# Optimization experiments

Hardware: AMD Instinct MI355X
Metric: run time of the kernel (lower is better)

Reference implementation:

```python
import jax, jax.numpy as jnp
import numpy as np

D = 64
H = 256


def _directions(d):
    """Taylor-coefficient directions matching Bilaplacian._set_up_taylor_coefficients."""
    eye = np.eye(d, dtype=np.float32)
    dirs1 = 4.0 * eye                                   # (D, D): 4*e_i
    pairs_neq = np.array([(i, j) for i in range(d) for j in range(d) if i != j])
    dirs2 = 3.0 * eye[pairs_neq[:, 0]] + eye[pairs_neq[:, 1]]      # (D(D-1), D): 3 e_i + e_j
    pairs_lt = np.array([(i, j) for i in range(d) for j in range(i + 1, d)])
    dirs3 = 2.0 * eye[pairs_lt[:, 0]] + 2.0 * eye[pairs_lt[:, 1]]  # (D(D-1)/2, D): 2 e_i + 2 e_j
    return jnp.asarray(dirs1), jnp.asarray(dirs2), jnp.asarray(dirs3)


def setup_inputs() -> dict:
    key = jax.random.key(0)
    ks = jax.random.split(key, 7)
    x = jax.random.normal(ks[0], (D,), dtype=jnp.float32)
    W1 = jax.random.normal(ks[1], (H, D), dtype=jnp.float32) / np.sqrt(D)
    b1 = 0.1 * jax.random.normal(ks[2], (H,), dtype=jnp.float32)
    W2 = jax.random.normal(ks[3], (H, H), dtype=jnp.float32) / np.sqrt(H)
    b2 = 0.1 * jax.random.normal(ks[4], (H,), dtype=jnp.float32)
    W3 = jax.random.normal(ks[5], (1, H), dtype=jnp.float32) / np.sqrt(H)
    b3 = 0.1 * jax.random.normal(ks[6], (1,), dtype=jnp.float32)
    return {"x": x, "W1": W1, "b1": b1, "W2": W2, "b2": b2, "W3": W3, "b3": b3}


def _bilaplacian(x, W1, b1, W2, b2, W3, b3):
    d = x.shape[0]

    def f(z):
        h = jnp.tanh(W1 @ z + b1)
        h = jnp.tanh(W2 @ h + b2)
        return W3 @ h + b3  # (1,)

    def d4(v):
        # 4th directional derivative d^4/dt^4 f(x + t v) via Taylor-mode (nested jvp)
        g1 = lambda z: jax.jvp(f, (z,), (v,))[1]
        g2 = lambda z: jax.jvp(g1, (z,), (v,))[1]
        g3 = lambda z: jax.jvp(g2, (z,), (v,))[1]
        return jax.jvp(g3, (x,), (v,))[1]

    dirs1, dirs2, dirs3 = _directions(d)
    S1 = jax.vmap(d4)(dirs1).sum(0)
    S2 = jax.vmap(d4)(dirs2).sum(0)
    S3 = jax.vmap(d4)(dirs3).sum(0)
    # Polarization weights s.t. alpha*S1 + beta*S2 + gamma*S3 = sum_{i,j} d^4 f / dx_i^2 dx_j^2
    alpha = (1.0 + 13.0 * (d - 1) / 9.0) / 256.0
    beta = -1.0 / 36.0
    gamma = 5.0 / 96.0
    return alpha * S1 + beta * S2 + gamma * S3


def reference(x, W1, b1, W2, b2, W3, b3):
    return _bilaplacian(x, W1, b1, W2, b2, W3, b3)
```

## Files before the change

kernel.cpp:

```cpp
#include <hip/hip_runtime.h>
#include <hip/hip_bf16.h>


#define C_F    0
#define H0_F   1024
#define R2_F   1280
#define E_F    1536
#define Q_F    2560
#define S5_F   2816
#define U_F    3072
#define S3_F   3328
#define S4_F   3584
#define P2_F   3840
#define G_F    4096
#define P_F    69632

__global__ __launch_bounds__(256) void k1_kernel(
    const float* __restrict__ x, const float* __restrict__ W1,
    const float* __restrict__ b1, float* __restrict__ ws_f, int* __restrict__ cnt) {
    __shared__ __align__(16) float smem[2 * 64 * 68];
    int tid = threadIdx.x, b = blockIdx.x;

    if (b == 0) {
        float* xs = smem;
        if (tid < 64) xs[tid] = x[tid];
        __syncthreads();
        const float4* row = (const float4*)(W1 + tid * 64);
        const float4* xv4 = (const float4*)xs;
        float u0 = b1[tid], r2v = 0.f;
        #pragma unroll
        for (int k = 0; k < 16; k++) {
            float4 w = row[k], xv = xv4[k];
            u0  += w.x * xv.x + w.y * xv.y + w.z * xv.z + w.w * xv.w;
            r2v += w.x * w.x + w.y * w.y + w.z * w.z + w.w * w.w;
        }
        float T = tanhf(u0), s = 1.f - T * T;
        ws_f[C_F + tid]       = s;
        ws_f[C_F + 256 + tid] = -2.f * T * s;
        ws_f[C_F + 512 + tid] = s * (6.f * T * T - 2.f);
        ws_f[C_F + 768 + tid] = s * T * (16.f - 24.f * T * T);
        ws_f[H0_F + tid] = T;
        ws_f[R2_F + tid] = r2v;
        ws_f[U_F  + tid] = 0.f;
        ws_f[S3_F + tid] = 0.f;
        ws_f[S4_F + tid] = 0.f;
        if (tid == 0) *cnt = 0;
    } else {
        int tb = b - 1, nb = tb >> 2, pb = tb & 3;
        float* As = smem;
        float* Bs = smem + 64 * 68;
        for (int idx = tid; idx < 4096; idx += 256) {
            int r = idx >> 6, i = idx & 63;
            As[i * 68 + r] = W1[(nb * 64 + r) * 64 + i];
            Bs[i * 68 + r] = W1[(pb * 64 + r) * 64 + i];
        }
        __syncthreads();
        int r0 = (tid & 15) * 4, c0 = (tid >> 4) * 4;
        float a[4][4] = {};
        for (int i = 0; i < 64; i++) {
            float4 av = *(const float4*)&As[i * 68 + r0];
            float4 bv = *(const float4*)&Bs[i * 68 + c0];
            float ar[4] = {av.x, av.y, av.z, av.w};
            float br[4] = {bv.x, bv.y, bv.z, bv.w};
            #pragma unroll
            for (int rr = 0; rr < 4; rr++)
                #pragma unroll
                for (int cc = 0; cc < 4; cc++)
                    a[rr][cc] = fmaf(ar[rr], br[cc], a[rr][cc]);
        }
        float* G = ws_f + G_F;
        #pragma unroll
        for (int rr = 0; rr < 4; rr++)
            #pragma unroll
            for (int cc = 0; cc < 4; cc++)
                G[(nb * 64 + r0 + rr) * 256 + pb * 64 + c0 + cc] = a[rr][cc];
    }
}

__global__ __launch_bounds__(256) void k2_kernel(
    const float* __restrict__ W1, const float* __restrict__ W2,
    const float* __restrict__ b2, const float* __restrict__ W3,
    float* __restrict__ ws_f) {
    __shared__ __align__(16) float smem[13248];
    int tid = threadIdx.x, b = blockIdx.x;
    const float* c1g = ws_f + C_F;
    const float* c2g = ws_f + C_F + 256;
    const float* c4g = ws_f + C_F + 768;

    if (b < 8) {
        int m0 = b * 32;
        float* Wc = smem;
        float* Bc = smem + 64 * 34;
        float acc2[2][4] = {};
        int tm2 = (tid & 15) * 2, ti = (tid >> 4) * 4;
        for (int nc = 0; nc < 4; nc++) {
            __syncthreads();
            for (int idx = tid; idx < 2048; idx += 256) {
                int mm = idx >> 6, nn = idx & 63;
                Wc[nn * 34 + mm] = W2[(m0 + mm) * 256 + nc * 64 + nn];
            }
            for (int idx = tid; idx < 4096; idx += 256) {
                int nn = idx >> 6, ii = idx & 63, n = nc * 64 + nn;
                Bc[nn * 68 + ii] = c1g[n] * W1[n * 64 + ii];
            }
            __syncthreads();
            for (int nn = 0; nn < 64; nn++) {
                float2 a2 = *(const float2*)&Wc[nn * 34 + tm2];
                float4 b4 = *(const float4*)&Bc[nn * 68 + ti];
                float br[4] = {b4.x, b4.y, b4.z, b4.w};
                #pragma unroll
                for (int j = 0; j < 4; j++) {
                    acc2[0][j] = fmaf(a2.x, br[j], acc2[0][j]);
                    acc2[1][j] = fmaf(a2.y, br[j], acc2[1][j]);
                }
            }
        }
        float* P = ws_f + P_F;
        float s0 = 0.f, s1 = 0.f;
        #pragma unroll
        for (int j = 0; j < 4; j++) {
            P[(m0 + tm2) * 64 + ti + j]     = acc2[0][j];
            P[(m0 + tm2 + 1) * 64 + ti + j] = acc2[1][j];
            s0 += acc2[0][j] * acc2[0][j];
            s1 += acc2[1][j] * acc2[1][j];
        }
        __syncthreads();
        float* red = smem;
        red[tm2 * 16 + (tid >> 4)]       = s0;
        red[(tm2 + 1) * 16 + (tid >> 4)] = s1;
        __syncthreads();
        if (tid < 32) {
            float p = 0.f;
            #pragma unroll
            for (int g = 0; g < 16; g++) p += red[tid * 16 + g];
            ws_f[P2_F + m0 + tid] = p;
        }
    } else if (b < 12) {
        int m0 = (b - 8) * 64;
        float* Ws   = smem;
        float* h0s  = smem + 4160;
        float* aqs  = h0s + 256;
        float* a5s  = aqs + 256;
        float* part = a5s + 256;
        float r2v = ws_f[R2_F + tid];
        h0s[tid] = ws_f[H0_F + tid];
        aqs[tid] = c2g[tid] * r2v;
        a5s[tid] = c4g[tid] * r2v * r2v;
        int mm = tid & 63, nq = tid >> 6;
        float pv = 0.f, pq = 0.f, p5 = 0.f;
        for (int nc = 0; nc < 4; nc++) {
            __syncthreads();
            for (int idx = tid; idx < 4096; idx += 256) {
                int m2 = idx >> 6, nn = idx & 63;
                Ws[nn * 65 + m2] = W2[(m0 + m2) * 256 + nc * 64 + nn];
            }
            __syncthreads();
            #pragma unroll
            for (int k = 0; k < 16; k++) {
                int nn = nq * 16 + k, n = nc * 64 + nn;
                float wv = Ws[nn * 65 + mm];
                pv = fmaf(wv, h0s[n], pv);
                pq = fmaf(wv, aqs[n], pq);
                p5 = fmaf(wv, a5s[n], p5);
            }
        }
        part[nq * 64 + mm]       = pv;
        part[256 + nq * 64 + mm] = pq;
        part[512 + nq * 64 + mm] = p5;
        __syncthreads();
        if (tid < 64) {
            int m = m0 + tid;
            float v  = b2[m] + part[tid] + part[64 + tid] + part[128 + tid] + part[192 + tid];
            float q  = part[256 + tid] + part[320 + tid] + part[384 + tid] + part[448 + tid];
            float s5 = part[512 + tid] + part[576 + tid] + part[640 + tid] + part[704 + tid];
            float T2 = tanhf(v), s2 = 1.f - T2 * T2, w3 = W3[m];
            float* E = ws_f + E_F;
            E[m]       = w3 * s2;
            E[256 + m] = -2.f * w3 * T2 * s2;
            E[512 + m] = w3 * s2 * (6.f * T2 * T2 - 2.f);
            E[768 + m] = w3 * s2 * T2 * (16.f - 24.f * T2 * T2);
            ws_f[Q_F + m]  = q;
            ws_f[S5_F + m] = s5;
        }
    } else {
        int tb = b - 12, kb = tb >> 2, mb = tb & 3;
        float* As  = smem;
        float* Bs  = smem + 4352;
        float* W2k = smem + 8704;
        float* c2k = smem + 13056;
        for (int idx = tid; idx < 4096; idx += 256) {
            int a_ = idx >> 6, b_ = idx & 63;
            W2k[a_ * 68 + b_] = W2[(mb * 64 + a_) * 256 + kb * 64 + b_];
        }
        if (tid < 64) c2k[tid] = c2g[kb * 64 + tid];
        int r0 = (tid & 15) * 4, c0 = (tid >> 4) * 4;
        float a[4][4] = {};
        const float* G = ws_f + G_F;
        for (int nc = 0; nc < 4; nc++) {
            __syncthreads();
            float c2v = c2g[nc * 64 + (tid & 63)];
            for (int idx = tid; idx < 4096; idx += 256) {
                int a_ = idx >> 6, b_ = idx & 63;
                float gv = G[(kb * 64 + a_) * 256 + nc * 64 + b_];
                As[b_ * 68 + a_] = c2v * gv * gv;
                Bs[b_ * 68 + a_] = W2[(mb * 64 + a_) * 256 + nc * 64 + b_];
            }
            __syncthreads();
            for (int nn = 0; nn < 64; nn++) {
                float4 av = *(const float4*)&As[nn * 68 + r0];
                float4 bv = *(const float4*)&Bs[nn * 68 + c0];
                float ar[4] = {av.x, av.y, av.z, av.w};
                float br[4] = {bv.x, bv.y, bv.z, bv.w};
                #pragma unroll
                for (int rr = 0; rr < 4; rr++)
                    #pragma unroll
                    for (int cc = 0; cc < 4; cc++)
                        a[rr][cc] = fmaf(ar[rr], br[cc], a[rr][cc]);
            }
        }
        #pragma unroll
        for (int cc = 0; cc < 4; cc++) {
            float up = 0.f;
            #pragma unroll
            for (int rr = 0; rr < 4; rr++)
                up += a[rr][cc] * c2k[r0 + rr] * W2k[(c0 + cc) * 68 + r0 + rr];
            up += __shfl_xor(up, 8, 16);
            up += __shfl_xor(up, 4, 16);
            up += __shfl_xor(up, 2, 16);
            up += __shfl_xor(up, 1, 16);
            if ((tid & 15) == 0)
                atomicAdd(&ws_f[U_F + mb * 64 + c0 + cc], up);
        }
    }
}

__global__ __launch_bounds__(256) void k3_kernel(
    const float* __restrict__ W1, const float* __restrict__ W2,
    float* __restrict__ ws_f, int* __restrict__ cnt, float* __restrict__ out) {
    __shared__ __align__(16) float smem[13248];
    __shared__ int isLast;
    __shared__ double dsum[4];
    int tid = threadIdx.x, b = blockIdx.x;
    int mb = b >> 2, nb = b & 3;
    float* As  = smem;
    float* Bs  = smem + 4352;
    float* W2s = smem + 8704;
    float* c2s = smem + 13056;
    float* c34 = smem + 13120;
    const float* P = ws_f + P_F;
    for (int idx = tid; idx < 4096; idx += 256) {
        int a_ = idx >> 6, b_ = idx & 63;
        As[b_ * 68 + a_]  = P[(mb * 64 + a_) * 64 + b_];
        Bs[b_ * 68 + a_]  = W1[(nb * 64 + a_) * 64 + b_];
        W2s[a_ * 68 + b_] = W2[(mb * 64 + a_) * 256 + nb * 64 + b_];
    }
    if (tid < 64) {
        int n = nb * 64 + tid;
        c2s[tid] = ws_f[C_F + 256 + n];
        c34[tid] = ws_f[C_F + 512 + n] * ws_f[R2_F + n];
    }
    __syncthreads();
    int m0t = (tid >> 4) * 4, n0t = (tid & 15) * 4;
    float a[4][4] = {};
    for (int ii = 0; ii < 64; ii++) {
        float4 av = *(const float4*)&As[ii * 68 + m0t];
        float4 bv = *(const float4*)&Bs[ii * 68 + n0t];
        float ar[4] = {av.x, av.y, av.z, av.w};
        float br[4] = {bv.x, bv.y, bv.z, bv.w};
        #pragma unroll
        for (int rr = 0; rr < 4; rr++)
            #pragma unroll
            for (int cc = 0; cc < 4; cc++)
                a[rr][cc] = fmaf(ar[rr], br[cc], a[rr][cc]);
    }
    #pragma unroll
    for (int rr = 0; rr < 4; rr++) {
        float s3p = 0.f, s4p = 0.f;
        #pragma unroll
        for (int cc = 0; cc < 4; cc++) {
            float wv = W2s[(m0t + rr) * 68 + n0t + cc];
            float t  = a[rr][cc];
            s3p = fmaf(c2s[n0t + cc] * wv, t * t, s3p);
            s4p = fmaf(c34[n0t + cc] * wv, t, s4p);
        }
        s3p += __shfl_xor(s3p, 8, 16); s4p += __shfl_xor(s4p, 8, 16);
        s3p += __shfl_xor(s3p, 4, 16); s4p += __shfl_xor(s4p, 4, 16);
        s3p += __shfl_xor(s3p, 2, 16); s4p += __shfl_xor(s4p, 2, 16);
        s3p += __shfl_xor(s3p, 1, 16); s4p += __shfl_xor(s4p, 1, 16);
        if ((tid & 15) == 0) {
            atomicAdd(&ws_f[S3_F + mb * 64 + m0t + rr], s3p);
            atomicAdd(&ws_f[S4_F + mb * 64 + m0t + rr], s4p);
        }
    }
    __threadfence();
    if (tid == 0) isLast = (atomicAdd(cnt, 1) == 15) ? 1 : 0;
    __syncthreads();
    if (isLast) {
        int m = tid;
        float s3m = atomicAdd(&ws_f[S3_F + m], 0.f);
        float s4m = atomicAdd(&ws_f[S4_F + m], 0.f);
        float p2 = ws_f[P2_F + m], q = ws_f[Q_F + m];
        float um = ws_f[U_F + m],  s5 = ws_f[S5_F + m];
        const float* E = ws_f + E_F;
        float y = E[768 + m] * p2 * p2
                + E[512 + m] * (2.f * q * p2 + 4.f * s3m)
                + E[256 + m] * (q * q + 2.f * um + 4.f * s4m)
                + E[m] * s5;
        double part = (double)y;
        for (int off = 32; off > 0; off >>= 1) part += __shfl_down(part, off, 64);
        if ((tid & 63) == 0) dsum[tid >> 6] = part;
        __syncthreads();
        if (tid == 0) out[0] = (float)(dsum[0] + dsum[1] + dsum[2] + dsum[3]);
    }
}

extern "C" void kernel_launch(void* const* d_in, const int* in_sizes, int n_in,
                              void* d_out, int out_size, void* d_ws, size_t ws_size,
                              hipStream_t stream) {
    const float* x  = (const float*)d_in[0];
    const float* W1 = (const float*)d_in[1];
    const float* b1 = (const float*)d_in[2];
    const float* W2 = (const float*)d_in[3];
    const float* b2 = (const float*)d_in[4];
    const float* W3 = (const float*)d_in[5];

    char* ws = (char*)d_ws;
    int*    cnt  = (int*)ws;
    float*  ws_f = (float*)(ws + 16);
    float*  out  = (float*)d_out;

    k1_kernel<<<17, 256, 0, stream>>>(x, W1, b1, ws_f, cnt);
    k2_kernel<<<28, 256, 0, stream>>>(W1, W2, b2, W3, ws_f);
    k3_kernel<<<16, 256, 0, stream>>>(W1, W2, ws_f, cnt, out);
}
```

Before: 104.6 us.

## Fuse three kernels into one cooperative kernel with grid syncs

Merges the three launches into a single cooperative kernel of 32 blocks that uses grid.sync between phases. The layer-1 tanh coefficients are recomputed locally in the blocks that need them, so the old first stage no longer has to finish before the second starts. The aim is to remove launch gaps and the first inter-kernel dependency. In exchange it pays cooperative-launch overhead and grid-wide barrier cost, and the final reduction now runs on a single fixed block after the last barrier.

Result: slower. 143.3 us (+37.1%).

```diff
diff --git a/kernel.cpp b/kernel.cpp
--- a/kernel.cpp
+++ b/kernel.cpp
@@ -1,9 +1,11 @@
 #include <hip/hip_runtime.h>
+#include <hip/hip_cooperative_groups.h>
 #include <hip/hip_bf16.h>
 
+namespace cg = cooperative_groups;
+
 
 #define C_F    0
-#define H0_F   1024
 #define R2_F   1280
 #define E_F    1536
 #define Q_F    2560
@@ -15,40 +17,20 @@
 #define G_F    4096
 #define P_F    69632
 
-__global__ __launch_bounds__(256) void k1_kernel(
-    const float* __restrict__ x, const float* __restrict__ W1,
-    const float* __restrict__ b1, float* __restrict__ ws_f, int* __restrict__ cnt) {
-    __shared__ __align__(16) float smem[2 * 64 * 68];
+__global__ __launch_bounds__(256) void fused_kernel(
+    const float* __restrict__ x,  const float* __restrict__ W1,
+    const float* __restrict__ b1, const float* __restrict__ W2,
+    const float* __restrict__ b2, const float* __restrict__ W3,
+    float* __restrict__ ws_f, float* __restrict__ out) {
+    cg::grid_group grid = cg::this_grid();
+    __shared__ __align__(16) float smem[13248];
+    __shared__ double dsum[4];
     int tid = threadIdx.x, b = blockIdx.x;
 
-    if (b == 0) {
-        float* xs = smem;
-        if (tid < 64) xs[tid] = x[tid];
-        __syncthreads();
-        const float4* row = (const float4*)(W1 + tid * 64);
-        const float4* xv4 = (const float4*)xs;
-        float u0 = b1[tid], r2v = 0.f;
-        #pragma unroll
-        for (int k = 0; k < 16; k++) {
-            float4 w = row[k], xv = xv4[k];
-            u0  += w.x * xv.x + w.y * xv.y + w.z * xv.z + w.w * xv.w;
-            r2v += w.x * w.x + w.y * w.y + w.z * w.z + w.w * w.w;
-        }
-        float T = tanhf(u0), s = 1.f - T * T;
-        ws_f[C_F + tid]       = s;
-        ws_f[C_F + 256 + tid] = -2.f * T * s;
-        ws_f[C_F + 512 + tid] = s * (6.f * T * T - 2.f);
-        ws_f[C_F + 768 + tid] = s * T * (16.f - 24.f * T * T);
-        ws_f[H0_F + tid] = T;
-        ws_f[R2_F + tid] = r2v;
-        ws_f[U_F  + tid] = 0.f;
-        ws_f[S3_F + tid] = 0.f;
-        ws_f[S4_F + tid] = 0.f;
-        if (tid == 0) *cnt = 0;
-    } else {
-        int tb = b - 1, nb = tb >> 2, pb = tb & 3;
+    if (b < 16) {
+        int nb = b >> 2, pb = b & 3;
         float* As = smem;
-        float* Bs = smem + 64 * 68;
+        float* Bs = smem + 4352;
         for (int idx = tid; idx < 4096; idx += 256) {
             int r = idx >> 6, i = idx & 63;
             As[i * 68 + r] = W1[(nb * 64 + r) * 64 + i];
@@ -74,23 +56,26 @@
             #pragma unroll
             for (int cc = 0; cc < 4; cc++)
                 G[(nb * 64 + r0 + rr) * 256 + pb * 64 + c0 + cc] = a[rr][cc];
-    }
-}
-
-__global__ __launch_bounds__(256) void k2_kernel(
-    const float* __restrict__ W1, const float* __restrict__ W2,
-    const float* __restrict__ b2, const float* __restrict__ W3,
-    float* __restrict__ ws_f) {
-    __shared__ __align__(16) float smem[13248];
-    int tid = threadIdx.x, b = blockIdx.x;
-    const float* c1g = ws_f + C_F;
-    const float* c2g = ws_f + C_F + 256;
-    const float* c4g = ws_f + C_F + 768;
-
-    if (b < 8) {
-        int m0 = b * 32;
-        float* Wc = smem;
-        float* Bc = smem + 64 * 34;
+    } else if (b < 24) {
+        int m0 = (b - 16) * 32;
+        float* Wc  = smem;
+        float* Bc  = smem + 2176;
+        float* c1s = smem + 6528;
+        float* xs  = smem + 6784;
+        if (tid < 64) xs[tid] = x[tid];
+        __syncthreads();
+        {
+            const float4* row = (const float4*)(W1 + tid * 64);
+            const float4* xv4 = (const float4*)xs;
+            float u0 = b1[tid];
+            #pragma unroll
+            for (int k = 0; k < 16; k++) {
+                float4 w = row[k], xv = xv4[k];
+                u0 += w.x * xv.x + w.y * xv.y + w.z * xv.z + w.w * xv.w;
+            }
+            float T = tanhf(u0);
+            c1s[tid] = 1.f - T * T;
+        }
         float acc2[2][4] = {};
         int tm2 = (tid & 15) * 2, ti = (tid >> 4) * 4;
         for (int nc = 0; nc < 4; nc++) {
@@ -101,7 +86,7 @@
             }
             for (int idx = tid; idx < 4096; idx += 256) {
                 int nn = idx >> 6, ii = idx & 63, n = nc * 64 + nn;
-                Bc[nn * 68 + ii] = c1g[n] * W1[n * 64 + ii];
+                Bc[nn * 68 + ii] = c1s[n] * W1[n * 64 + ii];
             }
             __syncthreads();
             for (int nn = 0; nn < 64; nn++) {
@@ -135,17 +120,33 @@
             for (int g = 0; g < 16; g++) p += red[tid * 16 + g];
             ws_f[P2_F + m0 + tid] = p;
         }
-    } else if (b < 12) {
-        int m0 = (b - 8) * 64;
+    } else if (b < 28) {
+        int m0 = (b - 24) * 64;
         float* Ws   = smem;
         float* h0s  = smem + 4160;
-        float* aqs  = h0s + 256;
-        float* a5s  = aqs + 256;
-        float* part = a5s + 256;
-        float r2v = ws_f[R2_F + tid];
-        h0s[tid] = ws_f[H0_F + tid];
-        aqs[tid] = c2g[tid] * r2v;
-        a5s[tid] = c4g[tid] * r2v * r2v;
+        float* aqs  = smem + 4416;
+        float* a5s  = smem + 4672;
+        float* part = smem + 4928;
+        float* xs   = smem + 5696;
+        if (tid < 64) xs[tid] = x[tid];
+        __syncthreads();
+        {
+            const float4* row = (const float4*)(W1 + tid * 64);
+            const float4* xv4 = (const float4*)xs;
+            float u0 = b1[tid], r2v = 0.f;
+            #pragma unroll
+            for (int k = 0; k < 16; k++) {
+                float4 w = row[k], xv = xv4[k];
+                u0  += w.x * xv.x + w.y * xv.y + w.z * xv.z + w.w * xv.w;
+                r2v += w.x * w.x + w.y * w.y + w.z * w.z + w.w * w.w;
+            }
+            float T = tanhf(u0), s = 1.f - T * T;
+            float c2 = -2.f * T * s;
+            float c4 = s * T * (16.f - 24.f * T * T);
+            h0s[tid] = T;
+            aqs[tid] = c2 * r2v;
+            a5s[tid] = c4 * r2v * r2v;
+        }
         int mm = tid & 63, nq = tid >> 6;
         float pv = 0.f, pq = 0.f, p5 = 0.f;
         for (int nc = 0; nc < 4; nc++) {
@@ -182,8 +183,35 @@
             ws_f[Q_F + m]  = q;
             ws_f[S5_F + m] = s5;
         }
-    } else {
-        int tb = b - 12, kb = tb >> 2, mb = tb & 3;
+    } else if (b == 28) {
+        float* xs = smem;
+        if (tid < 64) xs[tid] = x[tid];
+        __syncthreads();
+        const float4* row = (const float4*)(W1 + tid * 64);
+        const float4* xv4 = (const float4*)xs;
+        float u0 = b1[tid], r2v = 0.f;
+        #pragma unroll
+        for (int k = 0; k < 16; k++) {
+            float4 w = row[k], xv = xv4[k];
+            u0  += w.x * xv.x + w.y * xv.y + w.z * xv.z + w.w * xv.w;
+            r2v += w.x * w.x + w.y * w.y + w.z * w.z + w.w * w.w;
+        }
+        float T = tanhf(u0), s = 1.f - T * T;
+        ws_f[C_F + tid]       = s;
+        ws_f[C_F + 256 + tid] = -2.f * T * s;
+        ws_f[C_F + 512 + tid] = s * (6.f * T * T - 2.f);
+        ws_f[C_F + 768 + tid] = s * T * (16.f - 24.f * T * T);
+        ws_f[R2_F + tid] = r2v;
+        ws_f[U_F  + tid] = 0.f;
+        ws_f[S3_F + tid] = 0.f;
+        ws_f[S4_F + tid] = 0.f;
+    }
+    __threadfence();
+    grid.sync();
+
+    if (b < 16) {
+        int kb = b >> 2, mb = b & 3;
+        const float* c2g = ws_f + C_F + 256;
         float* As  = smem;
         float* Bs  = smem + 4352;
         float* W2k = smem + 8704;
@@ -231,76 +259,67 @@
             if ((tid & 15) == 0)
                 atomicAdd(&ws_f[U_F + mb * 64 + c0 + cc], up);
         }
-    }
-}
-
-__global__ __launch_bounds__(256) void k3_kernel(
-    const float* __restrict__ W1, const float* __restrict__ W2,
-    float* __restrict__ ws_f, int* __restrict__ cnt, float* __restrict__ out) {
-    __shared__ __align__(16) float smem[13248];
-    __shared__ int isLast;
-    __shared__ double dsum[4];
-    int tid = threadIdx.x, b = blockIdx.x;
-    int mb = b >> 2, nb = b & 3;
-    float* As  = smem;
-    float* Bs  = smem + 4352;
-    float* W2s = smem + 8704;
-    float* c2s = smem + 13056;
-    float* c34 = smem + 13120;
-    const float* P = ws_f + P_F;
-    for (int idx = tid; idx < 4096; idx += 256) {
-        int a_ = idx >> 6, b_ = idx & 63;
-        As[b_ * 68 + a_]  = P[(mb * 64 + a_) * 64 + b_];
-        Bs[b_ * 68 + a_]  = W1[(nb * 64 + a_) * 64 + b_];
-        W2s[a_ * 68 + b_] = W2[(mb * 64 + a_) * 256 + nb * 64 + b_];
-    }
-    if (tid < 64) {
-        int n = nb * 64 + tid;
-        c2s[tid] = ws_f[C_F + 256 + n];
-        c34[tid] = ws_f[C_F + 512 + n] * ws_f[R2_F + n];
-    }
-    __syncthreads();
-    int m0t = (tid >> 4) * 4, n0t = (tid & 15) * 4;
-    float a[4][4] = {};
-    for (int ii = 0; ii < 64; ii++) {
-        float4 av = *(const float4*)&As[ii * 68 + m0t];
-        float4 bv = *(const float4*)&Bs[ii * 68 + n0t];
-        float ar[4] = {av.x, av.y, av.z, av.w};
-        float br[4] = {bv.x, bv.y, bv.z, bv.w};
-        #pragma unroll
-        for (int rr = 0; rr < 4; rr++)
-            #pragma unroll
-            for (int cc = 0; cc < 4; cc++)
-                a[rr][cc] = fmaf(ar[rr], br[cc], a[rr][cc]);
-    }
-    #pragma unroll
-    for (int rr = 0; rr < 4; rr++) {
-        float s3p = 0.f, s4p = 0.f;
-        #pragma unroll
-        for (int cc = 0; cc < 4; cc++) {
-            float wv = W2s[(m0t + rr) * 68 + n0t + cc];
-            float t  = a[rr][cc];
-            s3p = fmaf(c2s[n0t + cc] * wv, t * t, s3p);
-            s4p = fmaf(c34[n0t + cc] * wv, t, s4p);
-        }
-        s3p += __shfl_xor(s3p, 8, 16); s4p += __shfl_xor(s4p, 8, 16);
-        s3p += __shfl_xor(s3p, 4, 16); s4p += __shfl_xor(s4p, 4, 16);
-        s3p += __shfl_xor(s3p, 2, 16); s4p += __shfl_xor(s4p, 2, 16);
-        s3p += __shfl_xor(s3p, 1, 16); s4p += __shfl_xor(s4p, 1, 16);
-        if ((tid & 15) == 0) {
-            atomicAdd(&ws_f[S3_F + mb * 64 + m0t + rr], s3p);
-            atomicAdd(&ws_f[S4_F + mb * 64 + m0t + rr], s4p);
+    } else {
+        int tb = b - 16, mb = tb >> 2, nb = tb & 3;
+        float* As  = smem;
+        float* Bs  = smem + 4352;
+        float* W2s = smem + 8704;
+        float* c2s = smem + 13056;
+        float* c34 = smem + 13120;
+        const float* P = ws_f + P_F;
+        for (int idx = tid; idx < 4096; idx += 256) {
+            int a_ = idx >> 6, b_ = idx & 63;
+            As[b_ * 68 + a_]  = P[(mb * 64 + a_) * 64 + b_];
+            Bs[b_ * 68 + a_]  = W1[(nb * 64 + a_) * 64 + b_];
+            W2s[a_ * 68 + b_] = W2[(mb * 64 + a_) * 256 + nb * 64 + b_];
+        }
+        if (tid < 64) {
+            int n = nb * 64 + tid;
+            c2s[tid] = ws_f[C_F + 256 + n];
+            c34[tid] = ws_f[C_F + 512 + n] * ws_f[R2_F + n];
+        }
+        __syncthreads();
+        int m0t = (tid >> 4) * 4, n0t = (tid & 15) * 4;
+        float a[4][4] = {};
+        for (int ii = 0; ii < 64; ii++) {
+            float4 av = *(const float4*)&As[ii * 68 + m0t];
+            float4 bv = *(const float4*)&Bs[ii * 68 + n0t];
+            float ar[4] = {av.x, av.y, av.z, av.w};
+            float br[4] = {bv.x, bv.y, bv.z, bv.w};
+            #pragma unroll
+            for (int rr = 0; rr < 4; rr++)
+                #pragma unroll
+                for (int cc = 0; cc < 4; cc++)
+                    a[rr][cc] = fmaf(ar[rr], br[cc], a[rr][cc]);
+        }
+        #pragma unroll
+        for (int rr = 0; rr < 4; rr++) {
+            float s3p = 0.f, s4p = 0.f;
+            #pragma unroll
+            for (int cc = 0; cc < 4; cc++) {
+                float wv = W2s[(m0t + rr) * 68 + n0t + cc];
+                float t  = a[rr][cc];
+                s3p = fmaf(c2s[n0t + cc] * wv, t * t, s3p);
+                s4p = fmaf(c34[n0t + cc] * wv, t, s4p);
+            }
+            s3p += __shfl_xor(s3p, 8, 16); s4p += __shfl_xor(s4p, 8, 16);
+            s3p += __shfl_xor(s3p, 4, 16); s4p += __shfl_xor(s4p, 4, 16);
+            s3p += __shfl_xor(s3p, 2, 16); s4p += __shfl_xor(s4p, 2, 16);
+            s3p += __shfl_xor(s3p, 1, 16); s4p += __shfl_xor(s4p, 1, 16);
+            if ((tid & 15) == 0) {
+                atomicAdd(&ws_f[S3_F + mb * 64 + m0t + rr], s3p);
+                atomicAdd(&ws_f[S4_F + mb * 64 + m0t + rr], s4p);
+            }
         }
     }
     __threadfence();
-    if (tid == 0) isLast = (atomicAdd(cnt, 1) == 15) ? 1 : 0;
-    __syncthreads();
-    if (isLast) {
+    grid.sync();
+
+    if (b == 0) {
         int m = tid;
-        float s3m = atomicAdd(&ws_f[S3_F + m], 0.f);
-        float s4m = atomicAdd(&ws_f[S4_F + m], 0.f);
-        float p2 = ws_f[P2_F + m], q = ws_f[Q_F + m];
-        float um = ws_f[U_F + m],  s5 = ws_f[S5_F + m];
+        float s3m = ws_f[S3_F + m], s4m = ws_f[S4_F + m];
+        float p2 = ws_f[P2_F + m],  q  = ws_f[Q_F + m];
+        float um = ws_f[U_F + m],   s5 = ws_f[S5_F + m];
         const float* E = ws_f + E_F;
         float y = E[768 + m] * p2 * p2
                 + E[512 + m] * (2.f * q * p2 + 4.f * s3m)
@@ -324,12 +343,11 @@
     const float* b2 = (const float*)d_in[4];
     const float* W3 = (const float*)d_in[5];
 
-    char* ws = (char*)d_ws;
-    int*    cnt  = (int*)ws;
-    float*  ws_f = (float*)(ws + 16);
-    float*  out  = (float*)d_out;
-
-    k1_kernel<<<17, 256, 0, stream>>>(x, W1, b1, ws_f, cnt);
-    k2_kernel<<<28, 256, 0, stream>>>(W1, W2, b2, W3, ws_f);
-    k3_kernel<<<16, 256, 0, stream>>>(W1, W2, ws_f, cnt, out);
+    float* ws_f = (float*)((char*)d_ws + 16);
+    float* out  = (float*)d_out;
+
+    void* args[] = {(void*)&x, (void*)&W1, (void*)&b1, (void*)&W2,
+                    (void*)&b2, (void*)&W3, (void*)&ws_f, (void*)&out};
+    hipLaunchCooperativeKernel((const void*)fused_kernel, dim3(32), dim3(256),
+                               args, 0, stream);
 }
```
